# Kernel optimization log

Hardware: AMD Instinct MI355X
Metric: run time of the kernel (lower is better)

## Reference

```python
import jax, jax.numpy as jnp
import numpy as np

B = 128      # trees per batch
D = 10       # tree depth (perfect binary tree)
L = 2 ** D   # leaves per tree
V = 50000    # vocab
E = 300      # embed size
C = 5        # num classes


def setup_inputs() -> dict:
    key = jax.random.key(0)
    k0, k1, k2, k3 = jax.random.split(key, 4)
    return {
        "word_ids": jax.random.randint(k0, (B, L), 0, V),
        "embedding": jax.random.normal(k1, (V, E), jnp.float32) * 0.02,
        "W_w": jax.random.normal(k2, (E, 2 * E), jnp.float32) * (1.0 / np.sqrt(2 * E)),
        "W_b": jnp.zeros((E,), jnp.float32),
        "P_w": jax.random.normal(k3, (C, E), jnp.float32) * (1.0 / np.sqrt(E)),
        "P_b": jnp.zeros((C,), jnp.float32),
    }


def reference(word_ids, embedding, W_w, W_b, P_w, P_b):
    # Leaf nodes: relu(Embedding(word))  -> [B, L, E]
    h = jax.nn.relu(embedding[word_ids])
    # projection of every node (torch Linear: x @ W.T + b)
    logits = [jnp.einsum("bne,ce->bnc", h, P_w) + P_b]
    # Combine same-depth sibling pairs level by level (D fixed levels).
    for _ in range(D):
        pair = jnp.concatenate([h[:, 0::2], h[:, 1::2]], axis=-1)  # [B, n/2, 2E]
        h = jax.nn.relu(jnp.einsum("bnf,ef->bne", pair, W_w) + W_b)  # [B, n/2, E]
        logits.append(jnp.einsum("bne,ce->bnc", h, P_w) + P_b)
    # All node logits, leaves first then each internal level up to the root.
    return jnp.concatenate(logits, axis=1)  # [B, 2L-1, C]
```

## Files before the change

### kernel.cpp

```cpp
#include <hip/hip_runtime.h>
#include <hip/hip_bf16.h>

#define B_ 128
#define D_ 10
#define L_ 1024
#define E_ 300
#define C_ 5
#define NODES 2047
#define HSTR 304
#define KP 608
#define NP 320
#define PK 320
#define LSTR 328
#define ASTR 616

typedef __attribute__((ext_vector_type(8))) short short8;
typedef __attribute__((ext_vector_type(4))) float f32x4;
typedef __hip_bfloat16 bf16;

__device__ __forceinline__ short f2bs(float v) {
  bf16 b = (bf16)v;
  return *reinterpret_cast<short*>(&b);
}

__device__ __forceinline__ short8 pack_relu(f32x4 v0, f32x4 v1) {
  short8 s;
#pragma unroll
  for (int j = 0; j < 4; j++) s[j] = f2bs(fmaxf(v0[j], 0.f));
#pragma unroll
  for (int j = 0; j < 4; j++) s[4 + j] = f2bs(fmaxf(v1[j], 0.f));
  return s;
}

__global__ __launch_bounds__(256) void prep_k(const float* __restrict__ Ww,
                                              const float* __restrict__ Pw,
                                              bf16* __restrict__ Wp,
                                              bf16* __restrict__ Pp,
                                              bf16* __restrict__ Pq) {
  int idx = blockIdx.x * 256 + threadIdx.x;
  if (idx < NP * KP) {
    int r = idx / KP, c = idx % KP;
    float v = 0.f;
    if (r < E_) {
      if (c < E_) v = Ww[r * 600 + c];
      else if (c >= HSTR && c < HSTR + E_) v = Ww[r * 600 + (c - 4)];
    }
    Wp[idx] = (bf16)v;
  }
  if (idx < 16 * PK) {
    int r = idx / PK, c = idx % PK;
    float v = (r < C_ && c < E_) ? Pw[r * E_ + c] : 0.f;
    Pp[idx] = (bf16)v;
  }
  if (idx < 2 * 16 * KP) {
    int p = idx / (16 * KP);
    int rem = idx % (16 * KP);
    int r = rem / KP, c = rem % KP;
    int e = c - p * HSTR;
    float v = (r < C_ && e >= 0 && e < E_) ? Pw[r * E_ + e] : 0.f;
    Pq[idx] = (bf16)v;
  }
}

__global__ __launch_bounds__(256) void fused_l1_k(
    const int* __restrict__ wid, const float* __restrict__ emb,
    const bf16* __restrict__ Wp, const float* __restrict__ Wb,
    const bf16* __restrict__ Pq, const bf16* __restrict__ Pp,
    const float* __restrict__ Pb, bf16* __restrict__ h1,
    float* __restrict__ out) {
  __shared__ short hsA[32][ASTR];
  int tid = threadIdx.x;
  int m0 = blockIdx.x * 32;

  for (int i = tid; i < 32 * 76; i += 256) {
    int r = i / 76, c = i % 76;
    int par = c >= 38;
    int e0 = (c - 38 * par) * 8;
    int word = wid[2 * (m0 + r) + par];
    const float* src = emb + (size_t)word * E_ + e0;
    f32x4 v0 = *(const f32x4*)src;
    f32x4 v1;
    if (e0 == 296) v1 = (f32x4){0.f, 0.f, 0.f, 0.f};
    else v1 = *(const f32x4*)(src + 4);
    *(short8*)&hsA[r][c * 8] = pack_relu(v0, v1);
  }
  __syncthreads();

  int w = tid >> 6, l = tid & 63, q = l & 15, half = l >> 4;
  int p = w >> 1, rtl = w & 1;

  f32x4 acc[2][5];
#pragma unroll
  for (int rt = 0; rt < 2; rt++)
#pragma unroll
    for (int nt = 0; nt < 5; nt++) acc[rt][nt] = (f32x4){0.f, 0.f, 0.f, 0.f};
  f32x4 pacc = (f32x4){0.f, 0.f, 0.f, 0.f};

  for (int ks = 0; ks < 19; ks++) {
    int k0 = ks * 32 + half * 8;
    short8 a0 = *(const short8*)&hsA[q][k0];
    short8 a1 = *(const short8*)&hsA[16 + q][k0];
    short8 pf = *(const short8*)(Pq + ((size_t)p * 16 + q) * KP + k0);
    short8 al = rtl ? a1 : a0;
    pacc = __builtin_amdgcn_mfma_f32_16x16x32_bf16(al, pf, pacc, 0, 0, 0);
#pragma unroll
    for (int nt = 0; nt < 5; nt++) {
      short8 bfr =
          *(const short8*)(Wp + ((size_t)w * 80 + nt * 16 + q) * KP + k0);
      acc[0][nt] =
          __builtin_amdgcn_mfma_f32_16x16x32_bf16(a0, bfr, acc[0][nt], 0, 0, 0);
      acc[1][nt] =
          __builtin_amdgcn_mfma_f32_16x16x32_bf16(a1, bfr, acc[1][nt], 0, 0, 0);
    }
  }
  __syncthreads();

  bf16(*hsO)[LSTR] = (bf16(*)[LSTR]) & hsA[0][0];
#pragma unroll
  for (int nt = 0; nt < 5; nt++) {
    int n = w * 80 + nt * 16 + q;
    float wb = (n < E_) ? Wb[n] : 0.f;
#pragma unroll
    for (int rt = 0; rt < 2; rt++)
#pragma unroll
      for (int j = 0; j < 4; j++) {
        int r = rt * 16 + half * 4 + j;
        hsO[r][n] = (bf16)fmaxf(acc[rt][nt][j] + wb, 0.f);
      }
  }
  if (q < C_) {
    float pb = Pb[q];
#pragma unroll
    for (int j = 0; j < 4; j++) {
      int mrow = m0 + rtl * 16 + half * 4 + j;
      int leaf = 2 * mrow + p;
      out[((size_t)(leaf >> 10) * NODES + (leaf & 1023)) * C_ + q] =
          pacc[j] + pb;
    }
  }
  __syncthreads();

  for (int i = tid; i < 32 * 38; i += 256) {
    int r = i / 38, c = i % 38;
    *(short8*)(h1 + (size_t)(m0 + r) * HSTR + c * 8) =
        *(const short8*)&hsO[r][c * 8];
  }
  if (w < 2) {
    f32x4 pc = (f32x4){0.f, 0.f, 0.f, 0.f};
#pragma unroll
    for (int ks = 0; ks < 10; ks++) {
      int k0 = ks * 32 + half * 8;
      short8 a = *(const short8*)&hsO[w * 16 + q][k0];
      short8 bfr = *(const short8*)(Pp + (size_t)q * PK + k0);
      pc = __builtin_amdgcn_mfma_f32_16x16x32_bf16(a, bfr, pc, 0, 0, 0);
    }
    if (q < C_) {
      float pb = Pb[q];
#pragma unroll
      for (int j = 0; j < 4; j++) {
        int m = m0 + w * 16 + half * 4 + j;
        out[((size_t)(m >> 9) * NODES + 1024 + (m & 511)) * C_ + q] =
            pc[j] + pb;
      }
    }
  }
}

__global__ __launch_bounds__(256) void combine_mfma_k(
    const bf16* __restrict__ h_in, const bf16* __restrict__ Wp,
    const float* __restrict__ Wb, const bf16* __restrict__ Pp,
    const float* __restrict__ Pb, bf16* __restrict__ h_out,
    float* __restrict__ out, int node_off, int nshift) {
  __shared__ bf16 hs[64][LSTR];
  int tid = threadIdx.x;
  int w = tid >> 6;
  int l = tid & 63;
  int q = l & 15;
  int half = l >> 4;
  size_t m0 = (size_t)blockIdx.x * 64;

  f32x4 acc[4][5];
#pragma unroll
  for (int rt = 0; rt < 4; rt++)
#pragma unroll
    for (int nt = 0; nt < 5; nt++) acc[rt][nt] = (f32x4){0.f, 0.f, 0.f, 0.f};

#pragma unroll 2
  for (int ks = 0; ks < 19; ks++) {
    int k0 = ks * 32 + half * 8;
    short8 a[4], b[5];
#pragma unroll
    for (int rt = 0; rt < 4; rt++)
      a[rt] = *(const short8*)(h_in + (m0 + rt * 16 + q) * KP + k0);
#pragma unroll
    for (int nt = 0; nt < 5; nt++)
      b[nt] = *(const short8*)(Wp + (size_t)(w * 80 + nt * 16 + q) * KP + k0);
#pragma unroll
    for (int rt = 0; rt < 4; rt++)
#pragma unroll
      for (int nt = 0; nt < 5; nt++)
        acc[rt][nt] = __builtin_amdgcn_mfma_f32_16x16x32_bf16(
            a[rt], b[nt], acc[rt][nt], 0, 0, 0);
  }

  float wb[5];
#pragma unroll
  for (int nt = 0; nt < 5; nt++) {
    int n = w * 80 + nt * 16 + q;
    wb[nt] = (n < E_) ? Wb[n] : 0.f;
  }
#pragma unroll
  for (int rt = 0; rt < 4; rt++)
#pragma unroll
    for (int nt = 0; nt < 5; nt++) {
      int n = w * 80 + nt * 16 + q;
#pragma unroll
      for (int j = 0; j < 4; j++) {
        int rl = rt * 16 + half * 4 + j;
        hs[rl][n] = (bf16)fmaxf(acc[rt][nt][j] + wb[nt], 0.f);
      }
    }
  __syncthreads();

  for (int i = tid; i < 64 * 38; i += 256) {
    int r = i / 38, c = i % 38;
    *(short8*)(h_out + (m0 + r) * HSTR + c * 8) = *(const short8*)&hs[r][c * 8];
  }

  f32x4 pacc = (f32x4){0.f, 0.f, 0.f, 0.f};
#pragma unroll
  for (int ks = 0; ks < 10; ks++) {
    short8 a = *(const short8*)(&hs[16 * w + q][ks * 32 + half * 8]);
    short8 b = *(const short8*)(Pp + (size_t)q * PK + ks * 32 + half * 8);
    pacc = __builtin_amdgcn_mfma_f32_16x16x32_bf16(a, b, pacc, 0, 0, 0);
  }
  if (q < C_) {
    float pb = Pb[q];
#pragma unroll
    for (int j = 0; j < 4; j++) {
      size_t m = m0 + w * 16 + half * 4 + j;
      size_t b_ = m >> nshift;
      size_t n = m & (((size_t)1 << nshift) - 1);
      out[((size_t)b_ * NODES + node_off + n) * C_ + q] = pacc[j] + pb;
    }
  }
}

__global__ __launch_bounds__(256) void tail_k(
    const bf16* __restrict__ h5, const bf16* __restrict__ Wp,
    const float* __restrict__ Wb, const bf16* __restrict__ Pp,
    const float* __restrict__ Pb, float* __restrict__ out) {
  __shared__ bf16 bufs[2][32][LSTR];
  int tid = threadIdx.x, b = blockIdx.x;
  int w = tid >> 6, l = tid & 63, q = l & 15, half = l >> 4;

  for (int i = tid; i < 32 * 38; i += 256) {
    int r = i / 38, c = i % 38;
    *(short8*)&bufs[0][r][c * 8] =
        *(const short8*)(h5 + ((size_t)b * 32 + r) * HSTR + c * 8);
  }
  __syncthreads();

  int p = 0, off = 2016, Mo = 16;
  for (int lev = 0; lev < 5; lev++) {
    f32x4 acc[5];
#pragma unroll
    for (int t = 0; t < 5; t++) acc[t] = (f32x4){0.f, 0.f, 0.f, 0.f};
    for (int ks = 0; ks < 19; ks++) {
      int k0 = ks * 32 + half * 8;
      int sel = k0 >= HSTR;
      int e0 = k0 - (sel ? HSTR : 0);
      short8 a = *(const short8*)&bufs[p][2 * q + sel][e0];
#pragma unroll
      for (int t = 0; t < 5; t++) {
        int nt = w + 4 * t;
        short8 bfr = *(const short8*)(Wp + ((size_t)nt * 16 + q) * KP + k0);
        acc[t] = __builtin_amdgcn_mfma_f32_16x16x32_bf16(a, bfr, acc[t], 0, 0, 0);
      }
    }
    __syncthreads();
#pragma unroll
    for (int t = 0; t < 5; t++) {
      int nt = w + 4 * t;
      int n = nt * 16 + q;
      float wb = (n < E_) ? Wb[n] : 0.f;
#pragma unroll
      for (int j = 0; j < 4; j++) {
        int r = half * 4 + j;
        bufs[p ^ 1][r][n] = (bf16)fmaxf(acc[t][j] + wb, 0.f);
      }
    }
    __syncthreads();
    if (w == 0) {
      f32x4 pc = (f32x4){0.f, 0.f, 0.f, 0.f};
#pragma unroll
      for (int ks = 0; ks < 10; ks++) {
        int k0 = ks * 32 + half * 8;
        short8 a = *(const short8*)&bufs[p ^ 1][q][k0];
        short8 bfr = *(const short8*)(Pp + (size_t)q * PK + k0);
        pc = __builtin_amdgcn_mfma_f32_16x16x32_bf16(a, bfr, pc, 0, 0, 0);
      }
      if (q < C_) {
        float pb = Pb[q];
#pragma unroll
        for (int j = 0; j < 4; j++) {
          int r = half * 4 + j;
          if (r < Mo)
            out[((size_t)b * NODES + off + r) * C_ + q] = pc[j] + pb;
        }
      }
    }
    p ^= 1;
    off += Mo;
    Mo >>= 1;
  }
}

extern "C" void kernel_launch(void* const* d_in, const int* in_sizes, int n_in,
                              void* d_out, int out_size, void* d_ws,
                              size_t ws_size, hipStream_t stream) {
  const int* wid = (const int*)d_in[0];
  const float* emb = (const float*)d_in[1];
  const float* Ww = (const float*)d_in[2];
  const float* Wb = (const float*)d_in[3];
  const float* Pw = (const float*)d_in[4];
  const float* Pb = (const float*)d_in[5];
  float* out = (float*)d_out;

  bf16* hA = (bf16*)d_ws;
  bf16* hB = hA + (size_t)B_ * 512 * HSTR;
  bf16* Wp = hB + (size_t)B_ * 256 * HSTR;
  bf16* Pp = Wp + (size_t)NP * KP;
  bf16* Pq = Pp + (size_t)16 * PK;

  prep_k<<<(NP * KP + 255) / 256, 256, 0, stream>>>(Ww, Pw, Wp, Pp, Pq);
  fused_l1_k<<<(B_ * 512) / 32, 256, 0, stream>>>(wid, emb, Wp, Wb, Pq, Pp, Pb,
                                                  hA, out);
  bf16* cur = hA;
  int node_off = 1536;
  for (int lev = 2; lev <= 5; lev++) {
    int n_half = L_ >> lev;
    int M = B_ * n_half;
    bf16* nxt = (lev & 1) ? hA : hB;
    combine_mfma_k<<<M / 64, 256, 0, stream>>>(cur, Wp, Wb, Pp, Pb, nxt, out,
                                               node_off, D_ - lev);
    node_off += n_half;
    cur = nxt;
  }
  tail_k<<<B_, 256, 0, stream>>>(cur, Wp, Wb, Pp, Pb, out);
}
```

Before: 212.3 us.

## Pre-convert full embedding table to bf16 and gather directly in level-1 kernel

The prep kernel now converts the entire 50000x300 fp32 embedding table into a relu'd bf16 table padded to stride 304. The first-level kernel then reads MFMA A fragments straight from that table via per-row word offsets instead of staging gathered fp32 rows through shared memory. That kernel also grows its tile from 32 to 64 rows, with each wave covering four row tiles and both leaf projections. The aim is to remove per-element conversion and the LDS staging pass from the gather. The cost is converting the whole vocabulary every call, about 60 MB of fp32 read, rather than only the 131k referenced rows.

```diff
diff --git a/kernel.cpp b/kernel.cpp
--- a/kernel.cpp
+++ b/kernel.cpp
@@ -12,7 +12,6 @@
 #define NP 320
 #define PK 320
 #define LSTR 328
-#define ASTR 616
 
 typedef __attribute__((ext_vector_type(8))) short short8;
 typedef __attribute__((ext_vector_type(4))) float f32x4;
@@ -32,12 +31,21 @@
   return s;
 }
 
-__global__ __launch_bounds__(256) void prep_k(const float* __restrict__ Ww,
-                                              const float* __restrict__ Pw,
-                                              bf16* __restrict__ Wp,
-                                              bf16* __restrict__ Pp,
-                                              bf16* __restrict__ Pq) {
+__global__ __launch_bounds__(256) void prep_k(
+    const float* __restrict__ emb, const float* __restrict__ Ww,
+    const float* __restrict__ Pw, bf16* __restrict__ T, bf16* __restrict__ Wp,
+    bf16* __restrict__ Pp, bf16* __restrict__ Pq, int V) {
   int idx = blockIdx.x * 256 + threadIdx.x;
+  int tchunks = V * 38;
+  if (idx < tchunks) {
+    int v = idx / 38, c = idx % 38;
+    const float* src = emb + (size_t)v * E_ + c * 8;
+    f32x4 v0 = *(const f32x4*)src;
+    f32x4 v1;
+    if (c == 37) v1 = (f32x4){0.f, 0.f, 0.f, 0.f};
+    else v1 = *(const f32x4*)(src + 4);
+    *(short8*)(T + (size_t)v * HSTR + c * 8) = pack_relu(v0, v1);
+  }
   if (idx < NP * KP) {
     int r = idx / KP, c = idx % KP;
     float v = 0.f;
@@ -63,105 +71,104 @@
 }
 
 __global__ __launch_bounds__(256) void fused_l1_k(
-    const int* __restrict__ wid, const float* __restrict__ emb,
+    const int* __restrict__ wid, const bf16* __restrict__ T,
     const bf16* __restrict__ Wp, const float* __restrict__ Wb,
     const bf16* __restrict__ Pq, const bf16* __restrict__ Pp,
     const float* __restrict__ Pb, bf16* __restrict__ h1,
     float* __restrict__ out) {
-  __shared__ short hsA[32][ASTR];
+  __shared__ bf16 hs[64][LSTR];
   int tid = threadIdx.x;
-  int m0 = blockIdx.x * 32;
-
-  for (int i = tid; i < 32 * 76; i += 256) {
-    int r = i / 76, c = i % 76;
-    int par = c >= 38;
-    int e0 = (c - 38 * par) * 8;
-    int word = wid[2 * (m0 + r) + par];
-    const float* src = emb + (size_t)word * E_ + e0;
-    f32x4 v0 = *(const f32x4*)src;
-    f32x4 v1;
-    if (e0 == 296) v1 = (f32x4){0.f, 0.f, 0.f, 0.f};
-    else v1 = *(const f32x4*)(src + 4);
-    *(short8*)&hsA[r][c * 8] = pack_relu(v0, v1);
-  }
-  __syncthreads();
-
   int w = tid >> 6, l = tid & 63, q = l & 15, half = l >> 4;
-  int p = w >> 1, rtl = w & 1;
-
-  f32x4 acc[2][5];
-#pragma unroll
-  for (int rt = 0; rt < 2; rt++)
+  int m0 = blockIdx.x * 64;
+
+  int off0[4], off1[4];
+#pragma unroll
+  for (int rt = 0; rt < 4; rt++) {
+    int mrow = m0 + rt * 16 + q;
+    off0[rt] = wid[2 * mrow] * HSTR;
+    off1[rt] = wid[2 * mrow + 1] * HSTR;
+  }
+  int lm = m0 + w * 16 + q;
+  int lb0 = wid[2 * lm] * HSTR;
+  int lb1 = wid[2 * lm + 1] * HSTR;
+
+  f32x4 acc[4][5];
+#pragma unroll
+  for (int rt = 0; rt < 4; rt++)
 #pragma unroll
     for (int nt = 0; nt < 5; nt++) acc[rt][nt] = (f32x4){0.f, 0.f, 0.f, 0.f};
-  f32x4 pacc = (f32x4){0.f, 0.f, 0.f, 0.f};
+  f32x4 pacc[2];
+  pacc[0] = pacc[1] = (f32x4){0.f, 0.f, 0.f, 0.f};
 
   for (int ks = 0; ks < 19; ks++) {
     int k0 = ks * 32 + half * 8;
-    short8 a0 = *(const short8*)&hsA[q][k0];
-    short8 a1 = *(const short8*)&hsA[16 + q][k0];
-    short8 pf = *(const short8*)(Pq + ((size_t)p * 16 + q) * KP + k0);
-    short8 al = rtl ? a1 : a0;
-    pacc = __builtin_amdgcn_mfma_f32_16x16x32_bf16(al, pf, pacc, 0, 0, 0);
+    int sel = k0 >= HSTR;
+    int e0 = sel ? k0 - HSTR : k0;
+    short8 a[4];
+#pragma unroll
+    for (int rt = 0; rt < 4; rt++)
+      a[rt] = *(const short8*)(T + (sel ? off1[rt] : off0[rt]) + e0);
+    short8 al = *(const short8*)(T + (sel ? lb1 : lb0) + e0);
+    short8 pq0 = *(const short8*)(Pq + (size_t)q * KP + k0);
+    short8 pq1 = *(const short8*)(Pq + (size_t)(16 + q) * KP + k0);
+    pacc[0] = __builtin_amdgcn_mfma_f32_16x16x32_bf16(al, pq0, pacc[0], 0, 0, 0);
+    pacc[1] = __builtin_amdgcn_mfma_f32_16x16x32_bf16(al, pq1, pacc[1], 0, 0, 0);
 #pragma unroll
     for (int nt = 0; nt < 5; nt++) {
-      short8 bfr =
-          *(const short8*)(Wp + ((size_t)w * 80 + nt * 16 + q) * KP + k0);
-      acc[0][nt] =
-          __builtin_amdgcn_mfma_f32_16x16x32_bf16(a0, bfr, acc[0][nt], 0, 0, 0);
-      acc[1][nt] =
-          __builtin_amdgcn_mfma_f32_16x16x32_bf16(a1, bfr, acc[1][nt], 0, 0, 0);
-    }
-  }
-  __syncthreads();
-
-  bf16(*hsO)[LSTR] = (bf16(*)[LSTR]) & hsA[0][0];
+      short8 b =
+          *(const short8*)(Wp + (size_t)(w * 80 + nt * 16 + q) * KP + k0);
+#pragma unroll
+      for (int rt = 0; rt < 4; rt++)
+        acc[rt][nt] = __builtin_amdgcn_mfma_f32_16x16x32_bf16(a[rt], b,
+                                                              acc[rt][nt], 0,
+                                                              0, 0);
+    }
+  }
+
 #pragma unroll
   for (int nt = 0; nt < 5; nt++) {
     int n = w * 80 + nt * 16 + q;
     float wb = (n < E_) ? Wb[n] : 0.f;
 #pragma unroll
-    for (int rt = 0; rt < 2; rt++)
+    for (int rt = 0; rt < 4; rt++)
 #pragma unroll
       for (int j = 0; j < 4; j++) {
-        int r = rt * 16 + half * 4 + j;
-        hsO[r][n] = (bf16)fmaxf(acc[rt][nt][j] + wb, 0.f);
+        int rl = rt * 16 + half * 4 + j;
+        hs[rl][n] = (bf16)fmaxf(acc[rt][nt][j] + wb, 0.f);
       }
   }
   if (q < C_) {
     float pb = Pb[q];
 #pragma unroll
-    for (int j = 0; j < 4; j++) {
-      int mrow = m0 + rtl * 16 + half * 4 + j;
-      int leaf = 2 * mrow + p;
-      out[((size_t)(leaf >> 10) * NODES + (leaf & 1023)) * C_ + q] =
-          pacc[j] + pb;
-    }
+    for (int p = 0; p < 2; p++)
+#pragma unroll
+      for (int j = 0; j < 4; j++) {
+        int leaf = 2 * (m0 + w * 16 + half * 4 + j) + p;
+        out[((size_t)(leaf >> 10) * NODES + (leaf & 1023)) * C_ + q] =
+            pacc[p][j] + pb;
+      }
   }
   __syncthreads();
 
-  for (int i = tid; i < 32 * 38; i += 256) {
+  for (int i = tid; i < 64 * 38; i += 256) {
     int r = i / 38, c = i % 38;
     *(short8*)(h1 + (size_t)(m0 + r) * HSTR + c * 8) =
-        *(const short8*)&hsO[r][c * 8];
-  }
-  if (w < 2) {
-    f32x4 pc = (f32x4){0.f, 0.f, 0.f, 0.f};
-#pragma unroll
-    for (int ks = 0; ks < 10; ks++) {
-      int k0 = ks * 32 + half * 8;
-      short8 a = *(const short8*)&hsO[w * 16 + q][k0];
-      short8 bfr = *(const short8*)(Pp + (size_t)q * PK + k0);
-      pc = __builtin_amdgcn_mfma_f32_16x16x32_bf16(a, bfr, pc, 0, 0, 0);
-    }
-    if (q < C_) {
-      float pb = Pb[q];
-#pragma unroll
-      for (int j = 0; j < 4; j++) {
-        int m = m0 + w * 16 + half * 4 + j;
-        out[((size_t)(m >> 9) * NODES + 1024 + (m & 511)) * C_ + q] =
-            pc[j] + pb;
-      }
+        *(const short8*)&hs[r][c * 8];
+  }
+  f32x4 pc = (f32x4){0.f, 0.f, 0.f, 0.f};
+#pragma unroll
+  for (int ks = 0; ks < 10; ks++) {
+    int k0 = ks * 32 + half * 8;
+    short8 a = *(const short8*)&hs[16 * w + q][k0];
+    short8 b = *(const short8*)(Pp + (size_t)q * PK + k0);
+    pc = __builtin_amdgcn_mfma_f32_16x16x32_bf16(a, b, pc, 0, 0, 0);
+  }
+  if (q < C_) {
+    float pb = Pb[q];
+#pragma unroll
+    for (int j = 0; j < 4; j++) {
+      int m = m0 + w * 16 + half * 4 + j;
+      out[((size_t)(m >> 9) * NODES + 1024 + (m & 511)) * C_ + q] = pc[j] + pb;
     }
   }
 }
@@ -275,7 +282,8 @@
       for (int t = 0; t < 5; t++) {
         int nt = w + 4 * t;
         short8 bfr = *(const short8*)(Wp + ((size_t)nt * 16 + q) * KP + k0);
-        acc[t] = __builtin_amdgcn_mfma_f32_16x16x32_bf16(a, bfr, acc[t], 0, 0, 0);
+        acc[t] =
+            __builtin_amdgcn_mfma_f32_16x16x32_bf16(a, bfr, acc[t], 0, 0, 0);
       }
     }
     __syncthreads();
@@ -305,8 +313,7 @@
 #pragma unroll
         for (int j = 0; j < 4; j++) {
           int r = half * 4 + j;
-          if (r < Mo)
-            out[((size_t)b * NODES + off + r) * C_ + q] = pc[j] + pb;
+          if (r < Mo) out[((size_t)b * NODES + off + r) * C_ + q] = pc[j] + pb;
         }
       }
     }
@@ -326,15 +333,19 @@
   const float* Pw = (const float*)d_in[4];
   const float* Pb = (const float*)d_in[5];
   float* out = (float*)d_out;
+  int V = in_sizes[1] / E_;
 
   bf16* hA = (bf16*)d_ws;
   bf16* hB = hA + (size_t)B_ * 512 * HSTR;
   bf16* Wp = hB + (size_t)B_ * 256 * HSTR;
   bf16* Pp = Wp + (size_t)NP * KP;
   bf16* Pq = Pp + (size_t)16 * PK;
-
-  prep_k<<<(NP * KP + 255) / 256, 256, 0, stream>>>(Ww, Pw, Wp, Pp, Pq);
-  fused_l1_k<<<(B_ * 512) / 32, 256, 0, stream>>>(wid, emb, Wp, Wb, Pq, Pp, Pb,
+  bf16* T = Pq + (size_t)2 * 16 * KP;
+
+  int tchunks = V * 38;
+  prep_k<<<(tchunks + 255) / 256, 256, 0, stream>>>(emb, Ww, Pw, T, Wp, Pp, Pq,
+                                                    V);
+  fused_l1_k<<<(B_ * 512) / 64, 256, 0, stream>>>(wid, T, Wp, Wb, Pq, Pp, Pb,
                                                   hA, out);
   bf16* cur = hA;
   int node_off = 1536;
```

Result: no change. 211.4 us (-0.4%).
